# Kernel optimization log

Hardware: AMD Instinct MI355X
Metric: run time of the kernel (lower is better)

Reference implementation:

```python
import jax, jax.numpy as jnp
import numpy as np

B, T, I, O, M = 64, 512, 256, 1024, 8
MS = O // M          # module_size
IM = I * M           # input_dim * num_modules


def setup_inputs() -> dict:
    key = jax.random.key(0)
    ks = jax.random.split(key, 6)
    s = 0.02
    return {
        "x": jax.random.normal(ks[0], (B, T, I), dtype=jnp.float32),
        "W_in": jax.random.normal(ks[1], (O, I), dtype=jnp.float32) * s,
        "b_in": jnp.zeros((O,), dtype=jnp.float32),
        "W_h": jax.random.normal(ks[2], (O, O), dtype=jnp.float32) * s,
        "W_ir": jax.random.normal(ks[3], (IM, I), dtype=jnp.float32) * s,
        "b_ir": jnp.zeros((IM,), dtype=jnp.float32),
        "W_hr": jax.random.normal(ks[4], (IM, IM), dtype=jnp.float32) * s,
        "module_periods": jnp.ones((M,), dtype=jnp.float32),
        "module_shifts": jnp.zeros((M,), dtype=jnp.float32),
    }


def reference(x, W_in, b_in, W_h, W_ir, b_ir, W_hr, module_periods, module_shifts):
    # x: [B, T, I]
    def step(carry, inp):
        h, x_pred = carry           # h: [B,O], x_pred: [B,IM]
        ti, xi = inp                # ti scalar float, xi: [B,I]
        acts = jnp.tanh(xi @ W_in.T + b_in + h @ W_h.T)            # [B,O]
        acts_rec = jnp.tanh(xi @ W_ir.T + b_ir + x_pred @ W_hr.T)  # [B,IM]
        m_xp = x_pred.reshape(B, M, I)
        # NOTE: nn.LogSoftmax() with no dim on a 3D tensor defaults to dim=0 (batch axis)
        surprisal = jax.nn.log_softmax(m_xp, axis=0) * xi[:, None, :]  # [B,M,I]
        mean_surprisal = surprisal.mean(-1)                            # [B,M]
        mp = mean_surprisal * module_periods                           # [B,M]
        gate = (jnp.sin(ti * mp + module_shifts) + 1.0) * 0.5          # [B,M]
        gate_full = jnp.repeat(gate, MS, axis=-1)                      # [B,O]
        y = (1.0 - gate_full) * acts + gate_full * h
        return (y, acts_rec), (y, mp)

    ts = jnp.arange(T, dtype=x.dtype)
    carry0 = (jnp.zeros((B, O), dtype=x.dtype), jnp.zeros((B, IM), dtype=x.dtype))
    (h_final, _), (ys, ps) = jax.lax.scan(step, carry0, (ts, jnp.swapaxes(x, 0, 1)))
    ys = jnp.swapaxes(ys, 0, 1)   # [B,T,O]
    ps = jnp.swapaxes(ps, 0, 1)   # [B,T,M]
    return ys, h_final, ps
```

## Files before the change

### kernel.cpp

```cpp
#include <hip/hip_runtime.h>
#include <hip/hip_fp16.h>

typedef _Float16 f16;
typedef f16 f16x8 __attribute__((ext_vector_type(8)));
typedef f16 f16x4 __attribute__((ext_vector_type(4)));
typedef float f32x4 __attribute__((ext_vector_type(4)));
typedef float f32x16 __attribute__((ext_vector_type(16)));

#define B_ 64
#define T_ 512
#define I_ 256
#define O_ 1024
#define M_ 8
#define IM_ 2048
#define NRECB 128
#define NB 192
#define THREADS 256

#define OFF_X16 16384ull
#define SZ_X16  16777216ull
#define OFF_XP4 (OFF_X16 + SZ_X16)
#define OFF_H2  (OFF_XP4 + 4ull * B_ * IM_ * 2)

#define RECF_D(rh) (1024 + (rh) * 256)
#define ACTF_D     1536

#define CMB_REC 147456
#define XPRAW   81920
#define CMB_ACT 114688
#define LSE_O   126976
#define PART_O  128000
#define GATE_O  129024
#define SMEM_SZ 159744

#define WAITV(N) asm volatile("s_waitcnt vmcnt(" #N ")" ::: "memory")
#define LGKM0    asm volatile("s_waitcnt lgkmcnt(0)" ::: "memory")
#define SCHEDB   __builtin_amdgcn_sched_barrier(0)
#define BARRIER  __builtin_amdgcn_s_barrier()

#define ISSUE_AX(BUF, P) asm volatile( \
    "global_load_dwordx4 %0, %8, off\n\t" \
    "global_load_dwordx4 %1, %8, off offset:32\n\t" \
    "global_load_dwordx4 %2, %8, off offset:64\n\t" \
    "global_load_dwordx4 %3, %8, off offset:96\n\t" \
    "global_load_dwordx4 %4, %8, off offset:128\n\t" \
    "global_load_dwordx4 %5, %8, off offset:160\n\t" \
    "global_load_dwordx4 %6, %8, off offset:192\n\t" \
    "global_load_dwordx4 %7, %8, off offset:224" \
    : "=&v"(abuf[BUF][0]), "=&v"(abuf[BUF][1]), "=&v"(abuf[BUF][2]), "=&v"(abuf[BUF][3]), \
      "=&v"(abuf[BUF][4]), "=&v"(abuf[BUF][5]), "=&v"(abuf[BUF][6]), "=&v"(abuf[BUF][7]) \
    : "v"(P) : "memory")

#define ISSUE_AS(BUF, P) asm volatile( \
    "global_load_dwordx4 %0, %8, off sc0 sc1\n\t" \
    "global_load_dwordx4 %1, %8, off offset:32 sc0 sc1\n\t" \
    "global_load_dwordx4 %2, %8, off offset:64 sc0 sc1\n\t" \
    "global_load_dwordx4 %3, %8, off offset:96 sc0 sc1\n\t" \
    "global_load_dwordx4 %4, %8, off offset:128 sc0 sc1\n\t" \
    "global_load_dwordx4 %5, %8, off offset:160 sc0 sc1\n\t" \
    "global_load_dwordx4 %6, %8, off offset:192 sc0 sc1\n\t" \
    "global_load_dwordx4 %7, %8, off offset:224 sc0 sc1" \
    : "=&v"(abuf[BUF][0]), "=&v"(abuf[BUF][1]), "=&v"(abuf[BUF][2]), "=&v"(abuf[BUF][3]), \
      "=&v"(abuf[BUF][4]), "=&v"(abuf[BUF][5]), "=&v"(abuf[BUF][6]), "=&v"(abuf[BUF][7]) \
    : "v"(P) : "memory")

#define ISSUE8P(ARR, P0,P1,P2,P3,P4,P5,P6,P7) asm volatile( \
    "global_load_dwordx4 %0, %8, off sc0 sc1\n\t" \
    "global_load_dwordx4 %1, %9, off sc0 sc1\n\t" \
    "global_load_dwordx4 %2, %10, off sc0 sc1\n\t" \
    "global_load_dwordx4 %3, %11, off sc0 sc1\n\t" \
    "global_load_dwordx4 %4, %12, off sc0 sc1\n\t" \
    "global_load_dwordx4 %5, %13, off sc0 sc1\n\t" \
    "global_load_dwordx4 %6, %14, off sc0 sc1\n\t" \
    "global_load_dwordx4 %7, %15, off sc0 sc1" \
    : "=&v"((ARR)[0]), "=&v"((ARR)[1]), "=&v"((ARR)[2]), "=&v"((ARR)[3]), \
      "=&v"((ARR)[4]), "=&v"((ARR)[5]), "=&v"((ARR)[6]), "=&v"((ARR)[7]) \
    : "v"(P0), "v"(P1), "v"(P2), "v"(P3), "v"(P4), "v"(P5), "v"(P6), "v"(P7) \
    : "memory")

#define CH(I, WN) do { \
    WAITV(WN); SCHEDB; \
    _Pragma("unroll") \
    for (int kb = 0; kb < 8; ++kb) { \
        f16x8 bf = *(const f16x8*)(smem + addrB[kb] + (I) * 256); \
        if (kb & 1) acc1 = __builtin_amdgcn_mfma_f32_32x32x16_f16(abuf[I][kb], bf, acc1, 0, 0, 0); \
        else        acc0 = __builtin_amdgcn_mfma_f32_32x32x16_f16(abuf[I][kb], bf, acc0, 0, 0, 0); \
    } \
} while (0)

__device__ __forceinline__ void st_coh_h(f16* p, float vf) {
    union { f16 h; short s; } u; u.h = (f16)vf;
    asm volatile("global_store_short %0, %1, off sc0 sc1" :: "v"(p), "v"((int)u.s) : "memory");
}

__device__ __forceinline__ float fast_tanh(float x) {
    float e = __expf(2.f * x);
    return 1.f - 2.f / (e + 1.f);
}

__device__ __forceinline__ int ld_flag(const unsigned* p) {
    int v;
    asm volatile("global_load_dword %0, %1, off sc0 sc1" : "=v"(v) : "v"(p) : "memory");
    WAITV(0);
    return v;
}
__device__ __forceinline__ void st_flag(unsigned* p, int v) {
    asm volatile("global_store_dword %0, %1, off sc0 sc1" :: "v"(p), "v"(v) : "memory");
}

__global__ void init_kernel(const float* __restrict__ x, char* __restrict__ ws) {
    const int gid = blockIdx.x * 256 + threadIdx.x;
    if (blockIdx.x == 0) {
        for (int i = threadIdx.x; i < 4096; i += 256) ((unsigned*)ws)[i] = 0u;
    }
    f16* x16 = (f16*)(ws + OFF_X16);
    const int NQ = T_ * B_ * (I_ / 4);
    for (int q = gid; q < NQ; q += 256 * 256) {
        int t = q >> 12;
        int rem = q & 4095;
        int b = rem >> 6;
        int k4 = rem & 63;
        f32x4 v = *(const f32x4*)(x + ((size_t)b * T_ + t) * I_ + k4 * 4);
        f16x4 h;
        h[0] = (f16)v[0]; h[1] = (f16)v[1]; h[2] = (f16)v[2]; h[3] = (f16)v[3];
        *(f16x4*)(x16 + ((size_t)t * B_ + b) * I_ + k4 * 4) = h;
    }
    f16x8 z = {0, 0, 0, 0, 0, 0, 0, 0};
    f16* xp0 = (f16*)(ws + OFF_XP4);
    for (int e = gid * 8; e < B_ * IM_; e += 256 * 256 * 8) *(f16x8*)(xp0 + e) = z;
    f16* h0 = (f16*)(ws + OFF_H2);
    for (int e = gid * 8; e < B_ * O_; e += 256 * 256 * 8) *(f16x8*)(h0 + e) = z;
}

__global__ __launch_bounds__(THREADS, 1) void cwrnn_kernel(
    const float* __restrict__ x, const float* __restrict__ W_in, const float* __restrict__ b_in,
    const float* __restrict__ W_h, const float* __restrict__ W_ir, const float* __restrict__ b_ir,
    const float* __restrict__ W_hr, const float* __restrict__ periods, const float* __restrict__ shifts,
    float* __restrict__ out, char* __restrict__ ws)
{
    __shared__ __align__(16) char smem[SMEM_SZ];

    unsigned* bar = (unsigned*)ws;
    const int blk = blockIdx.x, tid = threadIdx.x;
    const int lane = tid & 63, w = tid >> 6;
    const int col = lane & 31, g = lane >> 5;

    float* ys = out;
    float* hfin = out + (size_t)B_ * T_ * O_;
    float* ps = hfin + (size_t)B_ * O_;

    f16* const xpB = (f16*)(ws + OFF_XP4);
    f16* h2 = (f16*)(ws + OFF_H2);

    if (blk < NRECB) {
        const int cg = blk >> 1, rh = blk & 1;
        const int j0 = cg * 32;
        const int row0 = rh * 32;
        const int arow = row0 + col;
        {
            const int j = tid & 31;
            const float* ra = W_ir + (size_t)(j0 + j) * I_;
            const float* rb = W_hr + (size_t)(j0 + j) * IM_ - 256;
            for (int u = (tid >> 5); u < 288; u += 8) {
                int k0 = u * 8;
                const float* s = (k0 < 256) ? (ra + k0) : (rb + k0);
                f32x4 lo = *(const f32x4*)s;
                f32x4 hi = *(const f32x4*)(s + 4);
                f16x8 v;
                #pragma unroll
                for (int e = 0; e < 4; ++e) { v[e] = (f16)lo[e]; v[e + 4] = (f16)hi[e]; }
                *(f16x8*)(smem + j * 4608 + ((u ^ (j & 15)) << 4)) = v;
            }
        }
        const float bir = b_ir[j0 + col];
        LGKM0; BARRIER;

        const int c0k = (w == 0) ? 0 : (w == 1) ? 5 : (w == 2) ? 10 : 14;
        int addrB[8];
        #pragma unroll
        for (int kb = 0; kb < 8; ++kb)
            addrB[kb] = col * 4608 + ((((kb << 1) + g) ^ (col & 15)) << 4) + c0k * 256;

        const char* xrow0 = (const char*)(ws + OFF_X16) + (size_t)arow * 512 + g * 16;
        unsigned* myslot = bar + RECF_D(rh) + cg * 4;

        for (int t = 0; t < T_ - 1; ++t) {
            if (w == 0) {
                const unsigned* p = bar + RECF_D(rh) + lane * 4;
                while (__ballot(ld_flag(p) >= t) != ~0ull) __builtin_amdgcn_s_sleep(4);
            } else if (w == 1) {
                const unsigned* p = bar + ACTF_D + lane * 4;
                const int tgt = t - 2;
                while (__ballot(ld_flag(p) >= tgt) != ~0ull) __builtin_amdgcn_s_sleep(4);
            }
            BARRIER;
            const int bi = t & 3, bn = (t + 1) & 3;
            const f16* xpcur = xpB + (size_t)bi * B_ * IM_;
            f16* xpnxt = xpB + (size_t)bn * B_ * IM_;
            const char* sprow = (const char*)xpcur + (size_t)arow * 4096 + g * 16 - 512;
            const char* xrow = xrow0 + (size_t)t * 32768;

            f16x8 abuf[5][8];
            f32x16 acc0, acc1;
            #pragma unroll
            for (int r = 0; r < 16; ++r) { acc0[r] = 0.f; acc1[r] = 0.f; }

            if (w == 0) {
                ISSUE_AX(0, xrow); ISSUE_AX(1, (xrow + 256));
                ISSUE_AS(2, (sprow + 2 * 256)); ISSUE_AS(3, (sprow + 3 * 256)); ISSUE_AS(4, (sprow + 4 * 256));
                CH(0, 32); CH(1, 24); CH(2, 16); CH(3, 8); CH(4, 0);
            } else if (w == 1) {
                ISSUE_AS(0, (sprow + 5 * 256)); ISSUE_AS(1, (sprow + 6 * 256)); ISSUE_AS(2, (sprow + 7 * 256));
                ISSUE_AS(3, (sprow + 8 * 256)); ISSUE_AS(4, (sprow + 9 * 256));
                CH(0, 32); CH(1, 24); CH(2, 16); CH(3, 8); CH(4, 0);
            } else if (w == 2) {
                ISSUE_AS(0, (sprow + 10 * 256)); ISSUE_AS(1, (sprow + 11 * 256));
                ISSUE_AS(2, (sprow + 12 * 256)); ISSUE_AS(3, (sprow + 13 * 256));
                CH(0, 24); CH(1, 16); CH(2, 8); CH(3, 0);
            } else {
                ISSUE_AS(0, (sprow + 14 * 256)); ISSUE_AS(1, (sprow + 15 * 256));
                ISSUE_AS(2, (sprow + 16 * 256)); ISSUE_AS(3, (sprow + 17 * 256));
                CH(0, 24); CH(1, 16); CH(2, 8); CH(3, 0);
            }

            f32x16 accS;
            #pragma unroll
            for (int r = 0; r < 16; ++r) accS[r] = acc0[r] + acc1[r];
            if (w > 0) {
                char* cb = smem + CMB_REC + (w - 1) * 4096 + lane * 16;
                #pragma unroll
                for (int q = 0; q < 4; ++q) {
                    f32x4 v = { accS[q*4+0], accS[q*4+1], accS[q*4+2], accS[q*4+3] };
                    *(f32x4*)(cb + q * 1024) = v;
                }
            }
            LGKM0; BARRIER;
            if (w == 0) {
                #pragma unroll
                for (int wv = 0; wv < 3; ++wv) {
                    const char* cb = smem + CMB_REC + wv * 4096 + lane * 16;
                    #pragma unroll
                    for (int q = 0; q < 4; ++q) {
                        f32x4 v = *(const f32x4*)(cb + q * 1024);
                        accS[q*4+0] += v[0]; accS[q*4+1] += v[1];
                        accS[q*4+2] += v[2]; accS[q*4+3] += v[3];
                    }
                }
                #pragma unroll
                for (int r = 0; r < 16; ++r) {
                    int rloc = (r & 3) + ((r >> 2) << 3) + (g << 2);
                    st_coh_h(xpnxt + (size_t)(row0 + rloc) * IM_ + j0 + col, fast_tanh(accS[r] + bir));
                }
                WAITV(0);
                if (tid == 0) st_flag(myslot, t + 1);
            }
        }
    } else {
        const int a = blk - NRECB;
        const int colg = a >> 1, rh = a & 1;
        const int m = colg >> 2;
        const int o0 = colg * 32;
        const int row0 = rh * 32;
        const int arow = row0 + col;
        {
            const int j = tid & 31;
            const float* ra = W_in + (size_t)(o0 + j) * I_;
            const float* rb = W_h + (size_t)(o0 + j) * O_ - 256;
            for (int u = (tid >> 5); u < 160; u += 8) {
                int k0 = u * 8;
                const float* s = (k0 < 256) ? (ra + k0) : (rb + k0);
                f32x4 lo = *(const f32x4*)s;
                f32x4 hi = *(const f32x4*)(s + 4);
                f16x8 v;
                #pragma unroll
                for (int e = 0; e < 4; ++e) { v[e] = (f16)lo[e]; v[e + 4] = (f16)hi[e]; }
                *(f16x8*)(smem + j * 2560 + ((u ^ (j & 15)) << 4)) = v;
            }
        }
        const float bin = b_in[o0 + col];
        const float per = periods[m], shf = shifts[m];
        LGKM0; BARRIER;

        const int c0k = (w == 0) ? 0 : (w == 1) ? 3 : (w == 2) ? 6 : 8;
        int addrB[8];
        #pragma unroll
        for (int kb = 0; kb < 8; ++kb)
            addrB[kb] = col * 2560 + ((((kb << 1) + g) ^ (col & 15)) << 4) + c0k * 256;

        char* xp_raw = smem + XPRAW;
        float* lse_lds = (float*)(smem + LSE_O);
        float* part_lds = (float*)(smem + PART_O);
        float* gate_lds = (float*)(smem + GATE_O);

        const char* xrow0 = (const char*)(ws + OFF_X16) + (size_t)arow * 512 + g * 16;
        unsigned* myslot = bar + ACTF_D + (rh * 32 + colg) * 4;
        float hreg[16];
        #pragma unroll
        for (int r = 0; r < 16; ++r) hreg[r] = 0.f;

        const int s_ = tid - 128;
        const int cg2 = s_ & 31;
        const int r0s = (s_ >> 5) << 4;

        for (int t = 0; t < T_; ++t) {
            if (w == 0) {
                const unsigned* p = bar + RECF_D(0) + lane * 4;
                while (__ballot(ld_flag(p) >= t) != ~0ull) __builtin_amdgcn_s_sleep(4);
            } else if (w == 1) {
                const unsigned* p = bar + RECF_D(1) + lane * 4;
                while (__ballot(ld_flag(p) >= t) != ~0ull) __builtin_amdgcn_s_sleep(4);
            } else if (w == 2) {
                const unsigned* p = bar + ACTF_D + (rh * 32 + (lane & 31)) * 4;
                while (__ballot((lane < 32) ? (ld_flag(p) >= t) : 1) != ~0ull) __builtin_amdgcn_s_sleep(4);
            }
            BARRIER;
            const int bi = t & 3;
            const f16* xpcur = xpB + (size_t)bi * B_ * IM_;
            const f16* hcur = h2 + (size_t)(t & 1) * B_ * O_;
            f16* hnxt = h2 + (size_t)((t + 1) & 1) * B_ * O_;

            const char* sprow = (const char*)hcur + (size_t)arow * 2048 + g * 16 - 512;
            const char* xrow = xrow0 + (size_t)t * 32768;
            f16x8 abuf[3][8];
            f16x8 sregA[8], sregB[8];
            f32x16 acc0, acc1;
            #pragma unroll
            for (int r = 0; r < 16; ++r) { acc0[r] = 0.f; acc1[r] = 0.f; }

            if (w == 0) {
                ISSUE_AX(0, xrow); ISSUE_AX(1, (xrow + 256)); ISSUE_AS(2, (sprow + 2 * 256));
                CH(0, 16); CH(1, 8); CH(2, 0);
            } else if (w == 1) {
                ISSUE_AS(0, (sprow + 3 * 256)); ISSUE_AS(1, (sprow + 4 * 256)); ISSUE_AS(2, (sprow + 5 * 256));
                CH(0, 16); CH(1, 8); CH(2, 0);
            } else {
                const int ca = (w == 2) ? 6 : 8;
                ISSUE_AS(0, (sprow + ca * 256)); ISSUE_AS(1, (sprow + (ca + 1) * 256));
                const char* xb = (const char*)xpcur + (size_t)m * 512 + (size_t)cg2 * 16 + (size_t)r0s * 4096;
                ISSUE8P(sregA, xb, xb + 4096, xb + 2*4096, xb + 3*4096,
                               xb + 4*4096, xb + 5*4096, xb + 6*4096, xb + 7*4096);
                ISSUE8P(sregB, (xb + 8*4096), xb + 9*4096, xb + 10*4096, xb + 11*4096,
                               xb + 12*4096, xb + 13*4096, xb + 14*4096, xb + 15*4096);
                CH(0, 24); CH(1, 16);
                WAITV(0); SCHEDB;
                #pragma unroll
                for (int k = 0; k < 8; ++k) {
                    int b0 = r0s + k;
                    *(f16x8*)(xp_raw + (size_t)b0 * 512 + ((cg2 ^ (b0 & 7)) << 4)) = sregA[k];
                    int b1 = r0s + 8 + k;
                    *(f16x8*)(xp_raw + (size_t)b1 * 512 + ((cg2 ^ (b1 & 7)) << 4)) = sregB[k];
                }
            }

            f32x16 accS;
            #pragma unroll
            for (int r = 0; r < 16; ++r) accS[r] = acc0[r] + acc1[r];
            if (w > 0) {
                char* cb = smem + CMB_ACT + (w - 1) * 4096 + lane * 16;
                #pragma unroll
                for (int q = 0; q < 4; ++q) {
                    f32x4 v = { accS[q*4+0], accS[q*4+1], accS[q*4+2], accS[q*4+3] };
                    *(f32x4*)(cb + q * 1024) = v;
                }
            }
            LGKM0; BARRIER;
            {
                int i = tid;
                int gq = i >> 3, r2 = (i & 7) * 2;
                float s = 0.f;
                #pragma unroll 8
                for (int b = 0; b < B_; ++b)
                    s += __expf((float)*(const f16*)(xp_raw + b * 512 + ((gq ^ (b & 7)) << 4) + r2));
                lse_lds[i] = __logf(s);
            }
            if (w == 0) {
                #pragma unroll
                for (int wv = 0; wv < 3; ++wv) {
                    const char* cb = smem + CMB_ACT + wv * 4096 + lane * 16;
                    #pragma unroll
                    for (int q = 0; q < 4; ++q) {
                        f32x4 v = *(const f32x4*)(cb + q * 1024);
                        accS[q*4+0] += v[0]; accS[q*4+1] += v[1];
                        accS[q*4+2] += v[2]; accS[q*4+3] += v[3];
                    }
                }
            }
            LGKM0; BARRIER;
            {
                int b = tid >> 2, q = tid & 3;
                const float* xr = x + ((size_t)b * T_ + t) * I_ + q * 64;
                float s = 0.f;
                #pragma unroll
                for (int k = 0; k < 8; ++k) {
                    f16x8 xp8 = *(const f16x8*)(xp_raw + (size_t)b * 512 + ((((q << 3) + k) ^ (b & 7)) << 4));
                    f32x4 xa = *(const f32x4*)(xr + k * 8);
                    f32x4 xb2 = *(const f32x4*)(xr + k * 8 + 4);
                    #pragma unroll
                    for (int jj = 0; jj < 4; ++jj)
                        s += ((float)xp8[jj] - lse_lds[(q << 6) + (k << 3) + jj]) * xa[jj];
                    #pragma unroll
                    for (int jj = 0; jj < 4; ++jj)
                        s += ((float)xp8[jj + 4] - lse_lds[(q << 6) + (k << 3) + 4 + jj]) * xb2[jj];
                }
                part_lds[tid] = s;
            }
            LGKM0; BARRIER;
            if (tid < B_) {
                float s = part_lds[tid * 4] + part_lds[tid * 4 + 1] + part_lds[tid * 4 + 2] + part_lds[tid * 4 + 3];
                float mp = (s * (1.f / 256.f)) * per;
                gate_lds[tid] = 0.5f * (sinf((float)t * mp + shf) + 1.f);
                if ((a & 7) == 0) ps[((size_t)tid * T_ + t) * M_ + m] = mp;
            }
            LGKM0; BARRIER;
            if (w == 0) {
                #pragma unroll
                for (int r = 0; r < 16; ++r) {
                    int rloc = (r & 3) + ((r >> 2) << 3) + (g << 2);
                    int row = row0 + rloc;
                    float gt = gate_lds[row];
                    float av = fast_tanh(accS[r] + bin);
                    float y = (1.f - gt) * av + gt * hreg[r];
                    hreg[r] = y;
                    st_coh_h(hnxt + (size_t)row * O_ + o0 + col, y);
                    ys[((size_t)row * T_ + t) * O_ + o0 + col] = y;
                    if (t == T_ - 1) hfin[(size_t)row * O_ + o0 + col] = y;
                }
                WAITV(0);
                if (tid == 0) st_flag(myslot, t + 1);
            }
        }
    }
}

extern "C" void kernel_launch(void* const* d_in, const int* in_sizes, int n_in,
                              void* d_out, int out_size, void* d_ws, size_t ws_size,
                              hipStream_t stream) {
    const float* x    = (const float*)d_in[0];
    const float* W_in = (const float*)d_in[1];
    const float* b_in = (const float*)d_in[2];
    const float* W_h  = (const float*)d_in[3];
    const float* W_ir = (const float*)d_in[4];
    const float* b_ir = (const float*)d_in[5];
    const float* W_hr = (const float*)d_in[6];
    const float* per  = (const float*)d_in[7];
    const float* shf  = (const float*)d_in[8];

    hipLaunchKernelGGL(init_kernel, dim3(256), dim3(256), 0, stream,
                       x, (char*)d_ws);
    hipLaunchKernelGGL(cwrnn_kernel, dim3(NB), dim3(THREADS), 0, stream,
                       x, W_in, b_in, W_h, W_ir, b_ir, W_hr, per, shf,
                       (float*)d_out, (char*)d_ws);
}
```

Baseline: 5.484 ms.

## Add per-XCD leader barrier and relax coherence on shared-state loads

Blocks register their XCD ID at startup and one leader block per XCD polls the global per-step flags. It then issues an agent-scope acquire fence and publishes a per-XCD flag that the other blocks on that XCD poll. Shared-state loads drop the sc1 bit and rely on the leader's fence. The hidden-state ring grows from 2 to 4 buffers and sleep intervals are shorter. The aim is to cut cross-die polling traffic and uncached-load latency, at the cost of an extra hop through the leader and reliance on L2 coherence within an XCD.

Measured after the change: 5.427 ms. No clear change (-1.0%).

```diff
diff --git a/kernel.cpp b/kernel.cpp
--- a/kernel.cpp
+++ b/kernel.cpp
@@ -20,10 +20,14 @@
 #define OFF_X16 16384ull
 #define SZ_X16  16777216ull
 #define OFF_XP4 (OFF_X16 + SZ_X16)
-#define OFF_H2  (OFF_XP4 + 4ull * B_ * IM_ * 2)
+#define OFF_H4  (OFF_XP4 + 4ull * B_ * IM_ * 2)
 
 #define RECF_D(rh) (1024 + (rh) * 256)
 #define ACTF_D     1536
+#define XCDF_D(x)  (2048 + (x) * 16)
+#define NRC_D(x)   (2560 + (x) * 16)
+#define NAC_D(x)   (2688 + (x) * 16)
+#define REGC_D     2816
 
 #define CMB_REC 147456
 #define XPRAW   81920
@@ -31,12 +35,14 @@
 #define LSE_O   126976
 #define PART_O  128000
 #define GATE_O  129024
-#define SMEM_SZ 159744
+#define META_O  159744
+#define SMEM_SZ 159808
 
 #define WAITV(N) asm volatile("s_waitcnt vmcnt(" #N ")" ::: "memory")
 #define LGKM0    asm volatile("s_waitcnt lgkmcnt(0)" ::: "memory")
 #define SCHEDB   __builtin_amdgcn_sched_barrier(0)
 #define BARRIER  __builtin_amdgcn_s_barrier()
+#define ACQ_FENCE __builtin_amdgcn_fence(__ATOMIC_ACQUIRE, "agent")
 
 #define ISSUE_AX(BUF, P) asm volatile( \
     "global_load_dwordx4 %0, %8, off\n\t" \
@@ -51,28 +57,28 @@
       "=&v"(abuf[BUF][4]), "=&v"(abuf[BUF][5]), "=&v"(abuf[BUF][6]), "=&v"(abuf[BUF][7]) \
     : "v"(P) : "memory")
 
-#define ISSUE_AS(BUF, P) asm volatile( \
-    "global_load_dwordx4 %0, %8, off sc0 sc1\n\t" \
-    "global_load_dwordx4 %1, %8, off offset:32 sc0 sc1\n\t" \
-    "global_load_dwordx4 %2, %8, off offset:64 sc0 sc1\n\t" \
-    "global_load_dwordx4 %3, %8, off offset:96 sc0 sc1\n\t" \
-    "global_load_dwordx4 %4, %8, off offset:128 sc0 sc1\n\t" \
-    "global_load_dwordx4 %5, %8, off offset:160 sc0 sc1\n\t" \
-    "global_load_dwordx4 %6, %8, off offset:192 sc0 sc1\n\t" \
-    "global_load_dwordx4 %7, %8, off offset:224 sc0 sc1" \
+#define ISSUE_A0(BUF, P) asm volatile( \
+    "global_load_dwordx4 %0, %8, off sc0\n\t" \
+    "global_load_dwordx4 %1, %8, off offset:32 sc0\n\t" \
+    "global_load_dwordx4 %2, %8, off offset:64 sc0\n\t" \
+    "global_load_dwordx4 %3, %8, off offset:96 sc0\n\t" \
+    "global_load_dwordx4 %4, %8, off offset:128 sc0\n\t" \
+    "global_load_dwordx4 %5, %8, off offset:160 sc0\n\t" \
+    "global_load_dwordx4 %6, %8, off offset:192 sc0\n\t" \
+    "global_load_dwordx4 %7, %8, off offset:224 sc0" \
     : "=&v"(abuf[BUF][0]), "=&v"(abuf[BUF][1]), "=&v"(abuf[BUF][2]), "=&v"(abuf[BUF][3]), \
       "=&v"(abuf[BUF][4]), "=&v"(abuf[BUF][5]), "=&v"(abuf[BUF][6]), "=&v"(abuf[BUF][7]) \
     : "v"(P) : "memory")
 
-#define ISSUE8P(ARR, P0,P1,P2,P3,P4,P5,P6,P7) asm volatile( \
-    "global_load_dwordx4 %0, %8, off sc0 sc1\n\t" \
-    "global_load_dwordx4 %1, %9, off sc0 sc1\n\t" \
-    "global_load_dwordx4 %2, %10, off sc0 sc1\n\t" \
-    "global_load_dwordx4 %3, %11, off sc0 sc1\n\t" \
-    "global_load_dwordx4 %4, %12, off sc0 sc1\n\t" \
-    "global_load_dwordx4 %5, %13, off sc0 sc1\n\t" \
-    "global_load_dwordx4 %6, %14, off sc0 sc1\n\t" \
-    "global_load_dwordx4 %7, %15, off sc0 sc1" \
+#define ISSUE8P0(ARR, P0,P1,P2,P3,P4,P5,P6,P7) asm volatile( \
+    "global_load_dwordx4 %0, %8, off sc0\n\t" \
+    "global_load_dwordx4 %1, %9, off sc0\n\t" \
+    "global_load_dwordx4 %2, %10, off sc0\n\t" \
+    "global_load_dwordx4 %3, %11, off sc0\n\t" \
+    "global_load_dwordx4 %4, %12, off sc0\n\t" \
+    "global_load_dwordx4 %5, %13, off sc0\n\t" \
+    "global_load_dwordx4 %6, %14, off sc0\n\t" \
+    "global_load_dwordx4 %7, %15, off sc0" \
     : "=&v"((ARR)[0]), "=&v"((ARR)[1]), "=&v"((ARR)[2]), "=&v"((ARR)[3]), \
       "=&v"((ARR)[4]), "=&v"((ARR)[5]), "=&v"((ARR)[6]), "=&v"((ARR)[7]) \
     : "v"(P0), "v"(P1), "v"(P2), "v"(P3), "v"(P4), "v"(P5), "v"(P6), "v"(P7) \
@@ -106,6 +112,12 @@
 }
 __device__ __forceinline__ void st_flag(unsigned* p, int v) {
     asm volatile("global_store_dword %0, %1, off sc0 sc1" :: "v"(p), "v"(v) : "memory");
+}
+__device__ __forceinline__ unsigned ld_rlx(unsigned* p) {
+    return __hip_atomic_load(p, __ATOMIC_RELAXED, __HIP_MEMORY_SCOPE_AGENT);
+}
+__device__ __forceinline__ unsigned rmw_add(unsigned* p) {
+    return __hip_atomic_fetch_add(p, 1u, __ATOMIC_RELAXED, __HIP_MEMORY_SCOPE_AGENT);
 }
 
 __global__ void init_kernel(const float* __restrict__ x, char* __restrict__ ws) {
@@ -128,11 +140,17 @@
     f16x8 z = {0, 0, 0, 0, 0, 0, 0, 0};
     f16* xp0 = (f16*)(ws + OFF_XP4);
     for (int e = gid * 8; e < B_ * IM_; e += 256 * 256 * 8) *(f16x8*)(xp0 + e) = z;
-    f16* h0 = (f16*)(ws + OFF_H2);
+    f16* h0 = (f16*)(ws + OFF_H4);
     for (int e = gid * 8; e < B_ * O_; e += 256 * 256 * 8) *(f16x8*)(h0 + e) = z;
 }
 
 __global__ __launch_bounds__(THREADS, 1) void cwrnn_kernel(
+    const float* __restrict__ x, const float* __restrict__ W_in, const float* __restrict__ b_in,
+    const float* __restrict__ W_h, const float* __restrict__ b_ir_dummy_Wh_, const float* __restrict__ W_ir_,
+    const float* __restrict__ W_hr_, const float* __restrict__ periods, const float* __restrict__ shifts,
+    float* __restrict__ out, char* __restrict__ ws);
+
+__global__ __launch_bounds__(THREADS, 1) void cwrnn_main(
     const float* __restrict__ x, const float* __restrict__ W_in, const float* __restrict__ b_in,
     const float* __restrict__ W_h, const float* __restrict__ W_ir, const float* __restrict__ b_ir,
     const float* __restrict__ W_hr, const float* __restrict__ periods, const float* __restrict__ shifts,
@@ -150,9 +168,28 @@
     float* ps = hfin + (size_t)B_ * O_;
 
     f16* const xpB = (f16*)(ws + OFF_XP4);
-    f16* h2 = (f16*)(ws + OFF_H2);
-
-    if (blk < NRECB) {
+    f16* h4 = (f16*)(ws + OFF_H4);
+    const bool isREC = (blk < NRECB);
+
+    int* meta = (int*)(smem + META_O);
+    if (tid == 0) {
+        unsigned xcdv;
+        asm volatile("s_getreg_b32 %0, hwreg(HW_REG_XCC_ID)" : "=s"(xcdv));
+        xcdv &= 7u;
+        unsigned rnk = rmw_add(&bar[isREC ? NRC_D(xcdv) : NAC_D(xcdv)]);
+        WAITV(0);
+        rmw_add(&bar[REGC_D]);
+        while (ld_rlx(&bar[REGC_D]) < (unsigned)NB) __builtin_amdgcn_s_sleep(8);
+        meta[0] = (int)xcdv;
+        meta[1] = (int)rnk;
+        meta[2] = (int)ld_rlx(&bar[NRC_D(xcdv)]);
+    }
+    LGKM0; BARRIER;
+    const int xcd_ = meta[0], rank = meta[1], nRx = meta[2];
+    const bool leader = isREC ? (rank == 0) : (rank == 0 && nRx == 0);
+    unsigned* xcdfp = bar + XCDF_D(xcd_);
+
+    if (isREC) {
         const int cg = blk >> 1, rh = blk & 1;
         const int j0 = cg * 32;
         const int row0 = rh * 32;
@@ -185,15 +222,32 @@
         unsigned* myslot = bar + RECF_D(rh) + cg * 4;
 
         for (int t = 0; t < T_ - 1; ++t) {
-            if (w == 0) {
-                const unsigned* p = bar + RECF_D(rh) + lane * 4;
-                while (__ballot(ld_flag(p) >= t) != ~0ull) __builtin_amdgcn_s_sleep(4);
-            } else if (w == 1) {
-                const unsigned* p = bar + ACTF_D + lane * 4;
-                const int tgt = t - 2;
-                while (__ballot(ld_flag(p) >= tgt) != ~0ull) __builtin_amdgcn_s_sleep(4);
-            }
-            BARRIER;
+            if (leader) {
+                if (w == 0) {
+                    const unsigned* p = bar + RECF_D(0) + lane * 4;
+                    while (__ballot(ld_flag(p) >= t) != ~0ull) __builtin_amdgcn_s_sleep(2);
+                } else if (w == 1) {
+                    const unsigned* p = bar + RECF_D(1) + lane * 4;
+                    while (__ballot(ld_flag(p) >= t) != ~0ull) __builtin_amdgcn_s_sleep(2);
+                } else if (w == 2) {
+                    const unsigned* p = bar + ACTF_D + lane * 4;
+                    const int tgt = t - 2;
+                    while (__ballot(ld_flag(p) >= tgt) != ~0ull) __builtin_amdgcn_s_sleep(2);
+                }
+                BARRIER;
+                if (tid == 0) { ACQ_FENCE; WAITV(0); st_flag(xcdfp, t + 1); }
+                BARRIER;
+            } else {
+                if (w == 0) {
+                    const unsigned* p = xcdfp;
+                    while (__ballot(ld_flag(p) >= t + 1) != ~0ull) __builtin_amdgcn_s_sleep(2);
+                } else if (w == 1) {
+                    const unsigned* p = bar + ACTF_D + lane * 4;
+                    const int tgt = t - 2;
+                    while (__ballot(ld_flag(p) >= tgt) != ~0ull) __builtin_amdgcn_s_sleep(2);
+                }
+                BARRIER;
+            }
             const int bi = t & 3, bn = (t + 1) & 3;
             const f16* xpcur = xpB + (size_t)bi * B_ * IM_;
             f16* xpnxt = xpB + (size_t)bn * B_ * IM_;
@@ -207,19 +261,19 @@
 
             if (w == 0) {
                 ISSUE_AX(0, xrow); ISSUE_AX(1, (xrow + 256));
-                ISSUE_AS(2, (sprow + 2 * 256)); ISSUE_AS(3, (sprow + 3 * 256)); ISSUE_AS(4, (sprow + 4 * 256));
+                ISSUE_A0(2, (sprow + 2 * 256)); ISSUE_A0(3, (sprow + 3 * 256)); ISSUE_A0(4, (sprow + 4 * 256));
                 CH(0, 32); CH(1, 24); CH(2, 16); CH(3, 8); CH(4, 0);
             } else if (w == 1) {
-                ISSUE_AS(0, (sprow + 5 * 256)); ISSUE_AS(1, (sprow + 6 * 256)); ISSUE_AS(2, (sprow + 7 * 256));
-                ISSUE_AS(3, (sprow + 8 * 256)); ISSUE_AS(4, (sprow + 9 * 256));
+                ISSUE_A0(0, (sprow + 5 * 256)); ISSUE_A0(1, (sprow + 6 * 256)); ISSUE_A0(2, (sprow + 7 * 256));
+                ISSUE_A0(3, (sprow + 8 * 256)); ISSUE_A0(4, (sprow + 9 * 256));
                 CH(0, 32); CH(1, 24); CH(2, 16); CH(3, 8); CH(4, 0);
             } else if (w == 2) {
-                ISSUE_AS(0, (sprow + 10 * 256)); ISSUE_AS(1, (sprow + 11 * 256));
-                ISSUE_AS(2, (sprow + 12 * 256)); ISSUE_AS(3, (sprow + 13 * 256));
+                ISSUE_A0(0, (sprow + 10 * 256)); ISSUE_A0(1, (sprow + 11 * 256));
+                ISSUE_A0(2, (sprow + 12 * 256)); ISSUE_A0(3, (sprow + 13 * 256));
                 CH(0, 24); CH(1, 16); CH(2, 8); CH(3, 0);
             } else {
-                ISSUE_AS(0, (sprow + 14 * 256)); ISSUE_AS(1, (sprow + 15 * 256));
-                ISSUE_AS(2, (sprow + 16 * 256)); ISSUE_AS(3, (sprow + 17 * 256));
+                ISSUE_A0(0, (sprow + 14 * 256)); ISSUE_A0(1, (sprow + 15 * 256));
+                ISSUE_A0(2, (sprow + 16 * 256)); ISSUE_A0(3, (sprow + 17 * 256));
                 CH(0, 24); CH(1, 16); CH(2, 8); CH(3, 0);
             }
 
@@ -254,6 +308,18 @@
                 WAITV(0);
                 if (tid == 0) st_flag(myslot, t + 1);
             }
+        }
+        if (leader) {
+            const int tt = T_ - 1;
+            if (w == 0) {
+                const unsigned* p = bar + RECF_D(0) + lane * 4;
+                while (__ballot(ld_flag(p) >= tt) != ~0ull) __builtin_amdgcn_s_sleep(2);
+            } else if (w == 1) {
+                const unsigned* p = bar + RECF_D(1) + lane * 4;
+                while (__ballot(ld_flag(p) >= tt) != ~0ull) __builtin_amdgcn_s_sleep(2);
+            }
+            BARRIER;
+            if (tid == 0) { ACQ_FENCE; WAITV(0); st_flag(xcdfp, tt + 1); }
         }
     } else {
         const int a = blk - NRECB;
@@ -303,21 +369,34 @@
         const int r0s = (s_ >> 5) << 4;
 
         for (int t = 0; t < T_; ++t) {
-            if (w == 0) {
-                const unsigned* p = bar + RECF_D(0) + lane * 4;
-                while (__ballot(ld_flag(p) >= t) != ~0ull) __builtin_amdgcn_s_sleep(4);
-            } else if (w == 1) {
-                const unsigned* p = bar + RECF_D(1) + lane * 4;
-                while (__ballot(ld_flag(p) >= t) != ~0ull) __builtin_amdgcn_s_sleep(4);
-            } else if (w == 2) {
-                const unsigned* p = bar + ACTF_D + (rh * 32 + (lane & 31)) * 4;
-                while (__ballot((lane < 32) ? (ld_flag(p) >= t) : 1) != ~0ull) __builtin_amdgcn_s_sleep(4);
-            }
-            BARRIER;
+            if (leader) {
+                if (w == 0) {
+                    const unsigned* p = bar + RECF_D(0) + lane * 4;
+                    while (__ballot(ld_flag(p) >= t) != ~0ull) __builtin_amdgcn_s_sleep(2);
+                } else if (w == 1) {
+                    const unsigned* p = bar + RECF_D(1) + lane * 4;
+                    while (__ballot(ld_flag(p) >= t) != ~0ull) __builtin_amdgcn_s_sleep(2);
+                } else if (w == 2) {
+                    const unsigned* p = bar + ACTF_D + (rh * 32 + (lane & 31)) * 4;
+                    while (__ballot((lane < 32) ? (ld_flag(p) >= t) : 1) != ~0ull) __builtin_amdgcn_s_sleep(2);
+                }
+                BARRIER;
+                if (tid == 0) { ACQ_FENCE; WAITV(0); st_flag(xcdfp, t + 1); }
+                BARRIER;
+            } else {
+                if (w == 0) {
+                    const unsigned* p = xcdfp;
+                    while (__ballot(ld_flag(p) >= t + 1) != ~0ull) __builtin_amdgcn_s_sleep(2);
+                } else if (w == 1) {
+                    const unsigned* p = bar + ACTF_D + (rh * 32 + (lane & 31)) * 4;
+                    while (__ballot((lane < 32) ? (ld_flag(p) >= t) : 1) != ~0ull) __builtin_amdgcn_s_sleep(2);
+                }
+                BARRIER;
+            }
             const int bi = t & 3;
             const f16* xpcur = xpB + (size_t)bi * B_ * IM_;
-            const f16* hcur = h2 + (size_t)(t & 1) * B_ * O_;
-            f16* hnxt = h2 + (size_t)((t + 1) & 1) * B_ * O_;
+            const f16* hcur = h4 + (size_t)(t & 3) * B_ * O_;
+            f16* hnxt = h4 + (size_t)((t + 1) & 3) * B_ * O_;
 
             const char* sprow = (const char*)hcur + (size_t)arow * 2048 + g * 16 - 512;
             const char* xrow = xrow0 + (size_t)t * 32768;
@@ -328,18 +407,18 @@
             for (int r = 0; r < 16; ++r) { acc0[r] = 0.f; acc1[r] = 0.f; }
 
             if (w == 0) {
-                ISSUE_AX(0, xrow); ISSUE_AX(1, (xrow + 256)); ISSUE_AS(2, (sprow + 2 * 256));
+                ISSUE_AX(0, xrow); ISSUE_AX(1, (xrow + 256)); ISSUE_A0(2, (sprow + 2 * 256));
                 CH(0, 16); CH(1, 8); CH(2, 0);
             } else if (w == 1) {
-                ISSUE_AS(0, (sprow + 3 * 256)); ISSUE_AS(1, (sprow + 4 * 256)); ISSUE_AS(2, (sprow + 5 * 256));
+                ISSUE_A0(0, (sprow + 3 * 256)); ISSUE_A0(1, (sprow + 4 * 256)); ISSUE_A0(2, (sprow + 5 * 256));
                 CH(0, 16); CH(1, 8); CH(2, 0);
             } else {
                 const int ca = (w == 2) ? 6 : 8;
-                ISSUE_AS(0, (sprow + ca * 256)); ISSUE_AS(1, (sprow + (ca + 1) * 256));
+                ISSUE_A0(0, (sprow + ca * 256)); ISSUE_A0(1, (sprow + (ca + 1) * 256));
                 const char* xb = (const char*)xpcur + (size_t)m * 512 + (size_t)cg2 * 16 + (size_t)r0s * 4096;
-                ISSUE8P(sregA, xb, xb + 4096, xb + 2*4096, xb + 3*4096,
+                ISSUE8P0(sregA, xb, xb + 4096, xb + 2*4096, xb + 3*4096,
                                xb + 4*4096, xb + 5*4096, xb + 6*4096, xb + 7*4096);
-                ISSUE8P(sregB, (xb + 8*4096), xb + 9*4096, xb + 10*4096, xb + 11*4096,
+                ISSUE8P0(sregB, (xb + 8*4096), xb + 9*4096, xb + 10*4096, xb + 11*4096,
                                xb + 12*4096, xb + 13*4096, xb + 14*4096, xb + 15*4096);
                 CH(0, 24); CH(1, 16);
                 WAITV(0); SCHEDB;
@@ -447,7 +526,7 @@
 
     hipLaunchKernelGGL(init_kernel, dim3(256), dim3(256), 0, stream,
                        x, (char*)d_ws);
-    hipLaunchKernelGGL(cwrnn_kernel, dim3(NB), dim3(THREADS), 0, stream,
+    hipLaunchKernelGGL(cwrnn_main, dim3(NB), dim3(THREADS), 0, stream,
                        x, W_in, b_in, W_h, W_ir, b_ir, W_hr, per, shf,
                        (float*)d_out, (char*)d_ws);
 }
```

## Split flag polling across waves per data dependency and drop block barrier

Applied to the files above, without the earlier changes.

Each wave now polls only the producer flags covering the K-chunks it actually reads, one flag per lane, spinning without sleeps and without the following block-wide barrier. The hidden-state exchange buffer grows from a double to a quad ring so producers can run further ahead. The ys and h_final global stores are moved after the step flag is published, so consumers are signalled earlier. The aim is to cut per-step synchronisation latency on the serial recurrence, at the cost of busier polling traffic and more delicate correctness reasoning.

After: 5.308 ms. -3.2%, faster.

```diff
diff --git a/kernel.cpp b/kernel.cpp
--- a/kernel.cpp
+++ b/kernel.cpp
@@ -20,7 +20,7 @@
 #define OFF_X16 16384ull
 #define SZ_X16  16777216ull
 #define OFF_XP4 (OFF_X16 + SZ_X16)
-#define OFF_H2  (OFF_XP4 + 4ull * B_ * IM_ * 2)
+#define OFF_H4  (OFF_XP4 + 4ull * B_ * IM_ * 2)
 
 #define RECF_D(rh) (1024 + (rh) * 256)
 #define ACTF_D     1536
@@ -128,11 +128,11 @@
     f16x8 z = {0, 0, 0, 0, 0, 0, 0, 0};
     f16* xp0 = (f16*)(ws + OFF_XP4);
     for (int e = gid * 8; e < B_ * IM_; e += 256 * 256 * 8) *(f16x8*)(xp0 + e) = z;
-    f16* h0 = (f16*)(ws + OFF_H2);
+    f16* h0 = (f16*)(ws + OFF_H4);
     for (int e = gid * 8; e < B_ * O_; e += 256 * 256 * 8) *(f16x8*)(h0 + e) = z;
 }
 
-__global__ __launch_bounds__(THREADS, 1) void cwrnn_kernel(
+__global__ __launch_bounds__(THREADS, 1) void cwrnn_main(
     const float* __restrict__ x, const float* __restrict__ W_in, const float* __restrict__ b_in,
     const float* __restrict__ W_h, const float* __restrict__ W_ir, const float* __restrict__ b_ir,
     const float* __restrict__ W_hr, const float* __restrict__ periods, const float* __restrict__ shifts,
@@ -150,7 +150,7 @@
     float* ps = hfin + (size_t)B_ * O_;
 
     f16* const xpB = (f16*)(ws + OFF_XP4);
-    f16* h2 = (f16*)(ws + OFF_H2);
+    f16* h4 = (f16*)(ws + OFF_H4);
 
     if (blk < NRECB) {
         const int cg = blk >> 1, rh = blk & 1;
@@ -181,19 +181,23 @@
         for (int kb = 0; kb < 8; ++kb)
             addrB[kb] = col * 4608 + ((((kb << 1) + g) ^ (col & 15)) << 4) + c0k * 256;
 
+        unsigned* fp = bar + RECF_D(0);
+        int off = 1 << 20;
+        if (w == 0)      { if (lane < 12) { fp = bar + RECF_D(rh) + lane * 4; off = 0; } }
+        else if (w == 1) { if (lane < 20) { fp = bar + RECF_D(rh) + (12 + lane) * 4; off = 0; } }
+        else if (w == 2) { if (lane < 16) { fp = bar + RECF_D(rh) + (32 + lane) * 4; off = 0; }
+                           else if (lane < 48) { fp = bar + ACTF_D + (lane - 16) * 4; off = 2; } }
+        else             { if (lane < 16) { fp = bar + RECF_D(rh) + (48 + lane) * 4; off = 0; }
+                           else if (lane < 48) { fp = bar + ACTF_D + (lane + 16) * 4; off = 2; } }
+
         const char* xrow0 = (const char*)(ws + OFF_X16) + (size_t)arow * 512 + g * 16;
         unsigned* myslot = bar + RECF_D(rh) + cg * 4;
 
         for (int t = 0; t < T_ - 1; ++t) {
-            if (w == 0) {
-                const unsigned* p = bar + RECF_D(rh) + lane * 4;
-                while (__ballot(ld_flag(p) >= t) != ~0ull) __builtin_amdgcn_s_sleep(4);
-            } else if (w == 1) {
-                const unsigned* p = bar + ACTF_D + lane * 4;
-                const int tgt = t - 2;
-                while (__ballot(ld_flag(p) >= tgt) != ~0ull) __builtin_amdgcn_s_sleep(4);
-            }
-            BARRIER;
+            {
+                int v = ld_flag(fp);
+                while (__ballot(v >= t - off) != ~0ull) v = ld_flag(fp);
+            }
             const int bi = t & 3, bn = (t + 1) & 3;
             const f16* xpcur = xpB + (size_t)bi * B_ * IM_;
             f16* xpnxt = xpB + (size_t)bn * B_ * IM_;
@@ -292,6 +296,16 @@
         float* part_lds = (float*)(smem + PART_O);
         float* gate_lds = (float*)(smem + GATE_O);
 
+        unsigned* fp = bar + RECF_D(0);
+        int off = 1 << 20;
+        if (w == 0)      { if (lane < 4)  { fp = bar + ACTF_D + (rh * 32 + lane) * 4; off = 0; } }
+        else if (w == 1) { if (lane < 12) { fp = bar + ACTF_D + (rh * 32 + 4 + lane) * 4; off = 0; } }
+        else if (w == 2) { if (lane < 8)  { fp = bar + ACTF_D + (rh * 32 + 16 + lane) * 4; off = 0; }
+                           else if (lane < 24) { int i = lane - 8; fp = bar + RECF_D(i >> 3) + (m * 8 + (i & 7)) * 4; off = 0; } }
+        else             { if (lane < 8)  { fp = bar + ACTF_D + (rh * 32 + 24 + lane) * 4; off = 0; }
+                           else if (lane < 24) { int i = lane - 8; fp = bar + RECF_D(i >> 3) + (m * 8 + (i & 7)) * 4; off = 0; }
+                           else if (lane < 56) { fp = bar + ACTF_D + (rh * 32 + (lane - 24)) * 4; off = 2; } }
+
         const char* xrow0 = (const char*)(ws + OFF_X16) + (size_t)arow * 512 + g * 16;
         unsigned* myslot = bar + ACTF_D + (rh * 32 + colg) * 4;
         float hreg[16];
@@ -303,21 +317,14 @@
         const int r0s = (s_ >> 5) << 4;
 
         for (int t = 0; t < T_; ++t) {
-            if (w == 0) {
-                const unsigned* p = bar + RECF_D(0) + lane * 4;
-                while (__ballot(ld_flag(p) >= t) != ~0ull) __builtin_amdgcn_s_sleep(4);
-            } else if (w == 1) {
-                const unsigned* p = bar + RECF_D(1) + lane * 4;
-                while (__ballot(ld_flag(p) >= t) != ~0ull) __builtin_amdgcn_s_sleep(4);
-            } else if (w == 2) {
-                const unsigned* p = bar + ACTF_D + (rh * 32 + (lane & 31)) * 4;
-                while (__ballot((lane < 32) ? (ld_flag(p) >= t) : 1) != ~0ull) __builtin_amdgcn_s_sleep(4);
-            }
-            BARRIER;
+            {
+                int v = ld_flag(fp);
+                while (__ballot(v >= t - off) != ~0ull) v = ld_flag(fp);
+            }
             const int bi = t & 3;
             const f16* xpcur = xpB + (size_t)bi * B_ * IM_;
-            const f16* hcur = h2 + (size_t)(t & 1) * B_ * O_;
-            f16* hnxt = h2 + (size_t)((t + 1) & 1) * B_ * O_;
+            const f16* hcur = h4 + (size_t)(t & 3) * B_ * O_;
+            f16* hnxt = h4 + (size_t)((t + 1) & 3) * B_ * O_;
 
             const char* sprow = (const char*)hcur + (size_t)arow * 2048 + g * 16 - 512;
             const char* xrow = xrow0 + (size_t)t * 32768;
@@ -413,6 +420,7 @@
             }
             LGKM0; BARRIER;
             if (w == 0) {
+                float yv[16];
                 #pragma unroll
                 for (int r = 0; r < 16; ++r) {
                     int rloc = (r & 3) + ((r >> 2) << 3) + (g << 2);
@@ -420,13 +428,18 @@
                     float gt = gate_lds[row];
                     float av = fast_tanh(accS[r] + bin);
                     float y = (1.f - gt) * av + gt * hreg[r];
-                    hreg[r] = y;
+                    hreg[r] = y; yv[r] = y;
                     st_coh_h(hnxt + (size_t)row * O_ + o0 + col, y);
-                    ys[((size_t)row * T_ + t) * O_ + o0 + col] = y;
-                    if (t == T_ - 1) hfin[(size_t)row * O_ + o0 + col] = y;
                 }
                 WAITV(0);
                 if (tid == 0) st_flag(myslot, t + 1);
+                #pragma unroll
+                for (int r = 0; r < 16; ++r) {
+                    int rloc = (r & 3) + ((r >> 2) << 3) + (g << 2);
+                    int row = row0 + rloc;
+                    ys[((size_t)row * T_ + t) * O_ + o0 + col] = yv[r];
+                    if (t == T_ - 1) hfin[(size_t)row * O_ + o0 + col] = yv[r];
+                }
             }
         }
     }
@@ -447,7 +460,7 @@
 
     hipLaunchKernelGGL(init_kernel, dim3(256), dim3(256), 0, stream,
                        x, (char*)d_ws);
-    hipLaunchKernelGGL(cwrnn_kernel, dim3(NB), dim3(THREADS), 0, stream,
+    hipLaunchKernelGGL(cwrnn_main, dim3(NB), dim3(THREADS), 0, stream,
                        x, W_in, b_in, W_h, W_ir, b_ir, W_hr, per, shf,
                        (float*)d_out, (char*)d_ws);
 }
```
